# Kernel optimization log

Measured on AMD Instinct MI355X. Metric: run time of the kernel, lower is better.

Reference implementation:

```python
import jax, jax.numpy as jnp
import numpy as np

O_DIM = 16   # output_dim (number of output capsules)
H_POSE = 16  # h (pose/vector dim per capsule)
NUM_ROUTING = 3


def _squash(s):
    # norm over the pose dim (axis=2), matching torch _squash(dim=2)
    norm = jnp.linalg.norm(s, axis=2, keepdims=True)
    norm_sq = norm * norm
    return s / norm * (norm_sq / (1.0 + norm_sq))


def setup_inputs() -> dict:
    key = jax.random.key(0)
    k1, k2 = jax.random.split(key, 2)
    B, I, C, H, W = 8, 32, 8, 16, 16
    x = jax.random.normal(k1, (B, I, C, H, W), dtype=jnp.float32)
    # weight ~ N(0, 0.1): shape (I, C, O*h) (torch stores (I, C, O*h, 1, 1))
    weight = 0.1 * jax.random.normal(k2, (I, C, O_DIM * H_POSE), dtype=jnp.float32)
    # bias initialized to 0.1, shape (O, h, 1, 1)
    bias = jnp.full((O_DIM, H_POSE, 1, 1), 0.1, dtype=jnp.float32)
    return {"x": x, "weight": weight, "bias": bias}


def reference(x, weight, bias):
    B, I, C, H, W = x.shape
    O, h = O_DIM, H_POSE
    # votes[b,i,o*h,H,W] = sum_c x[b,i,c,H,W] * weight[i,c,o*h]
    votes = jnp.einsum('bichw,icm->bimhw', x, weight)
    votes = votes.reshape(B, I, O, h, H, W)

    logits = jnp.zeros((B, I, O, H, W), dtype=x.dtype)
    activation = None
    for i in range(NUM_ROUTING):
        route = jax.nn.softmax(logits, axis=2)  # softmax over output capsules O
        last = (i == NUM_ROUTING - 1)
        v = votes if last else jax.lax.stop_gradient(votes)
        # preactivate[b,o,h,H,W] = sum_i route * votes + bias
        preact = jnp.sum(route[:, :, :, None] * v, axis=1) + bias  # bias broadcasts (O,h,1,1)
        activation = _squash(preact)  # [B, O, h, H, W]
        if not last:
            # distances[b,i,o,H,W] = sum_h stop_grad(votes) * activation
            distances = jnp.sum(jax.lax.stop_gradient(votes) * activation[:, None], axis=3)
            logits = logits + distances
    return activation
```

## Files before the change

kernel.cpp:

```cpp
#include <hip/hip_runtime.h>
#include <math.h>


__device__ __forceinline__ float4 f4zero() { return make_float4(0.f, 0.f, 0.f, 0.f); }

__device__ __forceinline__ void fma4(float4& a, float s, const float4& q) {
    a.x = fmaf(s, q.x, a.x); a.y = fmaf(s, q.y, a.y);
    a.z = fmaf(s, q.z, a.z); a.w = fmaf(s, q.w, a.w);
}

__global__ __launch_bounds__(256, 2)
void caps_kernel(const float* __restrict__ x,
                 const float* __restrict__ wgt,
                 const float* __restrict__ bias,
                 float* __restrict__ out)
{
    __shared__ float s_route [4 * 512];
    __shared__ float s_logits[4 * 512];
    __shared__ float s_part  [16 * 256];
    __shared__ float s_act   [4 * 256];

    const int t   = threadIdx.x;
    const int w   = t >> 6;
    const int l   = t & 63;
    const int b   = blockIdx.x >> 6;
    const int hw0 = (blockIdx.x & 63) << 2;

    const float4 bias4 = ((const float4*)bias)[l];

    float4 v[8][4];
    {
        const float*  xb = x + (size_t)b * 65536 + hw0;
        const float4* w4 = (const float4*)wgt;
        #pragma unroll
        for (int ii = 0; ii < 8; ++ii) {
            const int i = __builtin_amdgcn_readfirstlane((w << 3) + ii);
            #pragma unroll
            for (int p = 0; p < 4; ++p) v[ii][p] = f4zero();
            #pragma unroll
            for (int c = 0; c < 8; ++c) {
                const float4 wv = w4[i * 512 + c * 64 + l];
                const float4 xv = *(const float4*)(xb + (i * 8 + c) * 256);
                fma4(v[ii][0], xv.x, wv);
                fma4(v[ii][1], xv.y, wv);
                fma4(v[ii][2], xv.z, wv);
                fma4(v[ii][3], xv.w, wv);
            }
        }
    }

    float4 actreg = f4zero();

    #pragma unroll
    for (int it = 0; it < 3; ++it) {
        float4 pre[4];
        if (it == 0) {
            #pragma unroll
            for (int p = 0; p < 4; ++p) {
                float4 s = v[0][p];
                #pragma unroll
                for (int ii = 1; ii < 8; ++ii) {
                    s.x += v[ii][p].x; s.y += v[ii][p].y;
                    s.z += v[ii][p].z; s.w += v[ii][p].w;
                }
                pre[p] = make_float4(s.x * 0.0625f, s.y * 0.0625f,
                                     s.z * 0.0625f, s.w * 0.0625f);
            }
        } else {
            const int base = w * 512 + (l >> 1) * 16 + (l & 1) * 8;
            const float4 la = *(const float4*)&s_logits[base];
            const float4 lb = *(const float4*)&s_logits[base + 4];
            float mx = fmaxf(fmaxf(fmaxf(la.x, la.y), fmaxf(la.z, la.w)),
                             fmaxf(fmaxf(lb.x, lb.y), fmaxf(lb.z, lb.w)));
            mx = fmaxf(mx, __shfl_xor(mx, 1));
            const float e0 = __expf(la.x - mx), e1 = __expf(la.y - mx);
            const float e2 = __expf(la.z - mx), e3 = __expf(la.w - mx);
            const float e4 = __expf(lb.x - mx), e5 = __expf(lb.y - mx);
            const float e6 = __expf(lb.z - mx), e7 = __expf(lb.w - mx);
            float sum = ((e0 + e1) + (e2 + e3)) + ((e4 + e5) + (e6 + e7));
            sum += __shfl_xor(sum, 1);
            const float inv = 1.f / sum;
            *(float4*)&s_route[base]     = make_float4(e0 * inv, e1 * inv, e2 * inv, e3 * inv);
            *(float4*)&s_route[base + 4] = make_float4(e4 * inv, e5 * inv, e6 * inv, e7 * inv);
            __syncthreads();

            #pragma unroll
            for (int p = 0; p < 4; ++p) pre[p] = f4zero();
            const int rb = w * 512 + (l >> 2);
            #pragma unroll
            for (int ii = 0; ii < 8; ++ii) {
                #pragma unroll
                for (int p = 0; p < 4; ++p) {
                    const float r = s_route[rb + p * 128 + ii * 16];
                    fma4(pre[p], r, v[ii][p]);
                }
            }
        }

        #pragma unroll
        for (int p = 0; p < 4; ++p)
            *(float4*)&s_part[(w * 4 + p) * 256 + 4 * l] = pre[p];
        __syncthreads();

        float4 acc = bias4;
        #pragma unroll
        for (int wp = 0; wp < 4; ++wp) {
            const float4 q = *(const float4*)&s_part[(wp * 4 + w) * 256 + 4 * l];
            acc.x += q.x; acc.y += q.y; acc.z += q.z; acc.w += q.w;
        }
        float sq = acc.x * acc.x + acc.y * acc.y + acc.z * acc.z + acc.w * acc.w;
        sq += __shfl_xor(sq, 1);
        sq += __shfl_xor(sq, 2);
        const float f = sqrtf(sq) / (1.f + sq);
        actreg = make_float4(acc.x * f, acc.y * f, acc.z * f, acc.w * f);

        if (it < 2) {
            *(float4*)&s_act[w * 256 + 4 * l] = actreg;
            __syncthreads();

            float dacc[8];
            #pragma unroll
            for (int ii = 0; ii < 8; ++ii) dacc[ii] = 0.f;
            #pragma unroll
            for (int p = 0; p < 4; ++p) {
                const float4 a = *(const float4*)&s_act[p * 256 + 4 * l];
                #pragma unroll
                for (int ii = 0; ii < 8; ++ii) {
                    float d = v[ii][p].x * a.x + v[ii][p].y * a.y
                            + v[ii][p].z * a.z + v[ii][p].w * a.w;
                    d += __shfl_xor(d, 1);
                    d += __shfl_xor(d, 2);
                    dacc[ii] = ((l & 3) == p) ? d : dacc[ii];
                }
            }
            const int lb2 = w * 512 + (l & 3) * 128 + (l >> 2);
            if (it == 0) {
                #pragma unroll
                for (int ii = 0; ii < 8; ++ii) s_logits[lb2 + ii * 16] = dacc[ii];
            } else {
                #pragma unroll
                for (int ii = 0; ii < 8; ++ii) s_logits[lb2 + ii * 16] += dacc[ii];
            }
            __syncthreads();
        }
    }

    *(float4*)&s_act[w * 256 + 4 * l] = actreg;
    __syncthreads();
    float4 o4;
    o4.x = s_act[t];
    o4.y = s_act[256 + t];
    o4.z = s_act[512 + t];
    o4.w = s_act[768 + t];
    *(float4*)(out + (size_t)b * 65536 + (size_t)t * 256 + hw0) = o4;
}

extern "C" void kernel_launch(void* const* d_in, const int* in_sizes, int n_in,
                              void* d_out, int out_size, void* d_ws, size_t ws_size,
                              hipStream_t stream) {
    const float* x    = (const float*)d_in[0];
    const float* wgt  = (const float*)d_in[1];
    const float* bias = (const float*)d_in[2];
    float* out = (float*)d_out;
    caps_kernel<<<dim3(512), dim3(256), 0, stream>>>(x, wgt, bias, out);
}
```

Before: 72.79 us.

## Split input capsules across 8 waves per block with padded per-wave LDS

Doubles the block to 512 threads so each wave holds votes for 4 input capsules instead of 8, halving per-thread register use and raising occupancy. Route/logit storage becomes per-wave with a padded stride, so the softmax and logit updates only need a wave-local LDS fence instead of a block-wide barrier. The cross-wave reduction now sums 8 partials in 4 waves while the other 4 idle, and relies on wave-local waitcnt fences being sufficient for correctness.

```diff
diff --git a/kernel.cpp b/kernel.cpp
--- a/kernel.cpp
+++ b/kernel.cpp
@@ -1,6 +1,9 @@
 #include <hip/hip_runtime.h>
 #include <math.h>
 
+
+#define PSTR 80
+#define WSTR (4 * PSTR)
 
 __device__ __forceinline__ float4 f4zero() { return make_float4(0.f, 0.f, 0.f, 0.f); }
 
@@ -9,15 +12,21 @@
     a.z = fmaf(s, q.z, a.z); a.w = fmaf(s, q.w, a.w);
 }
 
-__global__ __launch_bounds__(256, 2)
+__device__ __forceinline__ void wave_lds_fence() {
+    __builtin_amdgcn_sched_barrier(0);
+    asm volatile("s_waitcnt lgkmcnt(0)" ::: "memory");
+    __builtin_amdgcn_sched_barrier(0);
+}
+
+__global__ __launch_bounds__(512, 4)
 void caps_kernel(const float* __restrict__ x,
                  const float* __restrict__ wgt,
                  const float* __restrict__ bias,
                  float* __restrict__ out)
 {
-    __shared__ float s_route [4 * 512];
-    __shared__ float s_logits[4 * 512];
-    __shared__ float s_part  [16 * 256];
+    __shared__ float s_logits[8 * WSTR];
+    __shared__ float s_route [8 * WSTR];
+    __shared__ float s_part  [32 * 256];
     __shared__ float s_act   [4 * 256];
 
     const int t   = threadIdx.x;
@@ -28,13 +37,13 @@
 
     const float4 bias4 = ((const float4*)bias)[l];
 
-    float4 v[8][4];
+    float4 v[4][4];
     {
         const float*  xb = x + (size_t)b * 65536 + hw0;
         const float4* w4 = (const float4*)wgt;
         #pragma unroll
-        for (int ii = 0; ii < 8; ++ii) {
-            const int i = __builtin_amdgcn_readfirstlane((w << 3) + ii);
+        for (int ii = 0; ii < 4; ++ii) {
+            const int i = __builtin_amdgcn_readfirstlane((w << 2) + ii);
             #pragma unroll
             for (int p = 0; p < 4; ++p) v[ii][p] = f4zero();
             #pragma unroll
@@ -49,8 +58,6 @@
         }
     }
 
-    float4 actreg = f4zero();
-
     #pragma unroll
     for (int it = 0; it < 3; ++it) {
         float4 pre[4];
@@ -59,7 +66,7 @@
             for (int p = 0; p < 4; ++p) {
                 float4 s = v[0][p];
                 #pragma unroll
-                for (int ii = 1; ii < 8; ++ii) {
+                for (int ii = 1; ii < 4; ++ii) {
                     s.x += v[ii][p].x; s.y += v[ii][p].y;
                     s.z += v[ii][p].z; s.w += v[ii][p].w;
                 }
@@ -67,31 +74,28 @@
                                      s.z * 0.0625f, s.w * 0.0625f);
             }
         } else {
-            const int base = w * 512 + (l >> 1) * 16 + (l & 1) * 8;
+            const int base = w * WSTR + (l >> 4) * PSTR + ((l >> 2) & 3) * 16 + (l & 3) * 4;
             const float4 la = *(const float4*)&s_logits[base];
-            const float4 lb = *(const float4*)&s_logits[base + 4];
-            float mx = fmaxf(fmaxf(fmaxf(la.x, la.y), fmaxf(la.z, la.w)),
-                             fmaxf(fmaxf(lb.x, lb.y), fmaxf(lb.z, lb.w)));
+            float mx = fmaxf(fmaxf(la.x, la.y), fmaxf(la.z, la.w));
             mx = fmaxf(mx, __shfl_xor(mx, 1));
+            mx = fmaxf(mx, __shfl_xor(mx, 2));
             const float e0 = __expf(la.x - mx), e1 = __expf(la.y - mx);
             const float e2 = __expf(la.z - mx), e3 = __expf(la.w - mx);
-            const float e4 = __expf(lb.x - mx), e5 = __expf(lb.y - mx);
-            const float e6 = __expf(lb.z - mx), e7 = __expf(lb.w - mx);
-            float sum = ((e0 + e1) + (e2 + e3)) + ((e4 + e5) + (e6 + e7));
+            float sum = (e0 + e1) + (e2 + e3);
             sum += __shfl_xor(sum, 1);
+            sum += __shfl_xor(sum, 2);
             const float inv = 1.f / sum;
-            *(float4*)&s_route[base]     = make_float4(e0 * inv, e1 * inv, e2 * inv, e3 * inv);
-            *(float4*)&s_route[base + 4] = make_float4(e4 * inv, e5 * inv, e6 * inv, e7 * inv);
-            __syncthreads();
+            *(float4*)&s_route[base] = make_float4(e0 * inv, e1 * inv, e2 * inv, e3 * inv);
+            wave_lds_fence();
 
             #pragma unroll
             for (int p = 0; p < 4; ++p) pre[p] = f4zero();
-            const int rb = w * 512 + (l >> 2);
+            const int rb = w * WSTR + (l >> 2);
             #pragma unroll
-            for (int ii = 0; ii < 8; ++ii) {
+            for (int p = 0; p < 4; ++p) {
                 #pragma unroll
-                for (int p = 0; p < 4; ++p) {
-                    const float r = s_route[rb + p * 128 + ii * 16];
+                for (int ii = 0; ii < 4; ++ii) {
+                    const float r = s_route[rb + p * PSTR + ii * 16];
                     fma4(pre[p], r, v[ii][p]);
                 }
             }
@@ -99,33 +103,32 @@
 
         #pragma unroll
         for (int p = 0; p < 4; ++p)
-            *(float4*)&s_part[(w * 4 + p) * 256 + 4 * l] = pre[p];
+            *(float4*)&s_part[((w << 2) + p) * 256 + (l << 2)] = pre[p];
         __syncthreads();
 
-        float4 acc = bias4;
-        #pragma unroll
-        for (int wp = 0; wp < 4; ++wp) {
-            const float4 q = *(const float4*)&s_part[(wp * 4 + w) * 256 + 4 * l];
-            acc.x += q.x; acc.y += q.y; acc.z += q.z; acc.w += q.w;
+        if (w < 4) {
+            float4 acc = bias4;
+            #pragma unroll
+            for (int wp = 0; wp < 8; ++wp) {
+                const float4 q = *(const float4*)&s_part[((wp << 2) + w) * 256 + (l << 2)];
+                acc.x += q.x; acc.y += q.y; acc.z += q.z; acc.w += q.w;
+            }
+            float sq = acc.x * acc.x + acc.y * acc.y + acc.z * acc.z + acc.w * acc.w;
+            sq += __shfl_xor(sq, 1);
+            sq += __shfl_xor(sq, 2);
+            const float f = sqrtf(sq) / (1.f + sq);
+            *(float4*)&s_act[w * 256 + (l << 2)] =
+                make_float4(acc.x * f, acc.y * f, acc.z * f, acc.w * f);
         }
-        float sq = acc.x * acc.x + acc.y * acc.y + acc.z * acc.z + acc.w * acc.w;
-        sq += __shfl_xor(sq, 1);
-        sq += __shfl_xor(sq, 2);
-        const float f = sqrtf(sq) / (1.f + sq);
-        actreg = make_float4(acc.x * f, acc.y * f, acc.z * f, acc.w * f);
+        __syncthreads();
 
         if (it < 2) {
-            *(float4*)&s_act[w * 256 + 4 * l] = actreg;
-            __syncthreads();
-
-            float dacc[8];
-            #pragma unroll
-            for (int ii = 0; ii < 8; ++ii) dacc[ii] = 0.f;
+            float dacc[4] = {0.f, 0.f, 0.f, 0.f};
             #pragma unroll
             for (int p = 0; p < 4; ++p) {
-                const float4 a = *(const float4*)&s_act[p * 256 + 4 * l];
+                const float4 a = *(const float4*)&s_act[p * 256 + (l << 2)];
                 #pragma unroll
-                for (int ii = 0; ii < 8; ++ii) {
+                for (int ii = 0; ii < 4; ++ii) {
                     float d = v[ii][p].x * a.x + v[ii][p].y * a.y
                             + v[ii][p].z * a.z + v[ii][p].w * a.w;
                     d += __shfl_xor(d, 1);
@@ -133,26 +136,26 @@
                     dacc[ii] = ((l & 3) == p) ? d : dacc[ii];
                 }
             }
-            const int lb2 = w * 512 + (l & 3) * 128 + (l >> 2);
+            const int lb2 = w * WSTR + (l & 3) * PSTR + (l >> 2);
             if (it == 0) {
                 #pragma unroll
-                for (int ii = 0; ii < 8; ++ii) s_logits[lb2 + ii * 16] = dacc[ii];
+                for (int ii = 0; ii < 4; ++ii) s_logits[lb2 + ii * 16] = dacc[ii];
             } else {
                 #pragma unroll
-                for (int ii = 0; ii < 8; ++ii) s_logits[lb2 + ii * 16] += dacc[ii];
+                for (int ii = 0; ii < 4; ++ii) s_logits[lb2 + ii * 16] += dacc[ii];
             }
-            __syncthreads();
+            wave_lds_fence();
         }
     }
 
-    *(float4*)&s_act[w * 256 + 4 * l] = actreg;
-    __syncthreads();
-    float4 o4;
-    o4.x = s_act[t];
-    o4.y = s_act[256 + t];
-    o4.z = s_act[512 + t];
-    o4.w = s_act[768 + t];
-    *(float4*)(out + (size_t)b * 65536 + (size_t)t * 256 + hw0) = o4;
+    if (t < 256) {
+        float4 o4;
+        o4.x = s_act[t];
+        o4.y = s_act[256 + t];
+        o4.z = s_act[512 + t];
+        o4.w = s_act[768 + t];
+        *(float4*)(out + (size_t)b * 65536 + (size_t)t * 256 + hw0) = o4;
+    }
 }
 
 extern "C" void kernel_launch(void* const* d_in, const int* in_sizes, int n_in,
@@ -162,5 +165,5 @@
     const float* wgt  = (const float*)d_in[1];
     const float* bias = (const float*)d_in[2];
     float* out = (float*)d_out;
-    caps_kernel<<<dim3(512), dim3(256), 0, stream>>>(x, wgt, bias, out);
+    caps_kernel<<<dim3(512), dim3(512), 0, stream>>>(x, wgt, bias, out);
 }
```

Result: no change. 71.45 us (-1.8%).
